# Kernel tuning notes

Hardware: AMD Instinct MI355X
Metric: run time of the kernel (lower is better)

Reference implementation:

```python
import jax, jax.numpy as jnp
import numpy as np

E = 4          # num_experts
B = 32         # batch
CIN = 64
COUT = 64
H = 112
WID = 112
K = 3          # kernel size


def setup_inputs() -> dict:
    key = jax.random.key(0)
    k1, k2, k3, k4 = jax.random.split(key, 4)
    x = jax.random.normal(k1, (B, CIN, H, WID), dtype=jnp.float32)
    layer_mask = jax.random.uniform(k2, (B, E), dtype=jnp.float32)
    # per-expert conv weights/biases (kaiming-ish scale)
    W = jax.random.normal(k3, (E, COUT, CIN, K, K), dtype=jnp.float32) * 0.05
    b = jax.random.normal(k4, (E, COUT), dtype=jnp.float32) * 0.05
    return {"x": x, "layer_mask": layer_mask, "W": W, "b": b}


def _conv(x, w):
    # stride 1, padding 1 on both spatial dims (matches nn.Conv2d(k=3, s=1, p=1))
    return jax.lax.conv_general_dilated(
        x, w, window_strides=(1, 1), padding=[(1, 1), (1, 1)],
        dimension_numbers=("NCHW", "OIHW", "NCHW"))


def reference(x, layer_mask, W, b):
    # Loop over the small fixed expert set, accumulating the gated sum to
    # avoid materializing an [E, B, C, H, W] intermediate.
    out = jnp.zeros((B, COUT, H, WID), dtype=x.dtype)
    for e in range(E):
        expert_out = _conv(x, W[e]) + b[e][None, :, None, None]
        gate = layer_mask[:, e][:, None, None, None]  # [B,1,1,1]
        out = out + expert_out * gate
    return out
```

## Files before the change

### kernel.cpp

```cpp
#include <hip/hip_runtime.h>
#include <stdint.h>

#define CIN   64
#define COUT  64
#define HH    112
#define WW    112
#define NEXP  4
#define HW    (HH * WW)

typedef short bf16x8 __attribute__((ext_vector_type(8)));
typedef float f32x16 __attribute__((ext_vector_type(16)));

__device__ inline uint16_t f2bf(float f) {
    uint32_t u = __builtin_bit_cast(uint32_t, f);
    return (uint16_t)((u + 0x7FFFu + ((u >> 16) & 1u)) >> 16);
}

__global__ __launch_bounds__(256)
void fold_wb(const float* __restrict__ W, const float* __restrict__ bias,
             const float* __restrict__ mask,
             uint16_t* __restrict__ Weff, float* __restrict__ Beff, int B) {
    int idx = blockIdx.x * 256 + threadIdx.x;
    if (idx >= B * 72 * 512) return;
    int j   = idx & 7;
    int co  = (idx >> 3) & 63;
    int g   = (idx >> 9) % 72;
    int n   = idx / (512 * 72);
    int par   = g & 1;
    int kq    = (g >> 1) & 1;
    int khw   = (g >> 2) % 9;
    int phase = (g >> 2) / 9;
    int ci = phase * 32 + (kq * 2 + par) * 8 + j;
    float acc = 0.f;
#pragma unroll
    for (int e = 0; e < NEXP; ++e)
        acc = fmaf(mask[n * NEXP + e],
                   W[((size_t)(e * COUT + co) * CIN + ci) * 9 + khw], acc);
    Weff[idx] = f2bf(acc);
    if (g == 0 && j == 0) {
        float ba = 0.f;
#pragma unroll
        for (int e = 0; e < NEXP; ++e)
            ba = fmaf(mask[n * NEXP + e], bias[e * COUT + co], ba);
        Beff[n * COUT + co] = ba;
    }
}

__global__ __launch_bounds__(256, 3)
void conv_fused(const float* __restrict__ x, const uint16_t* __restrict__ Weff,
                const float* __restrict__ Beff, float* __restrict__ out,
                int nwg) {
    __shared__ uint16_t ldsx[324 * 32];

    int bid = blockIdx.x;
    if ((nwg & 7) == 0)
        bid = (bid & 7) * (nwg >> 3) + (bid >> 3);

    const int tid  = threadIdx.x;
    const int lane = tid & 63;
    const int wid  = tid >> 6;
    const int tileIdx = bid % 49;
    const int n  = bid / 49;
    const int th = tileIdx / 7, tw = tileIdx % 7;
    const int h0 = th * 16, w0 = tw * 16;

    const int rowb = wid * 4 + ((lane & 31) >> 4);
    const int colb = lane & 15;
    const int par  = lane >> 5;

    const uint16_t* wbase = Weff + (size_t)n * 36864
                          + (size_t)par * 512 + (size_t)(lane & 31) * 8;

    f32x16 acc00 = {}, acc01 = {}, acc10 = {}, acc11 = {};

#pragma unroll
    for (int phase = 0; phase < 2; ++phase) {
        if (phase) __syncthreads();
        for (int u = tid; u < 1296; u += 256) {
            int s   = u & 3;
            int pix = u >> 2;
            int dh = pix / 18, dw = pix - dh * 18;
            int h = h0 + dh - 1, w = w0 + dw - 1;
            int cg = s ^ ((pix >> 1) & 3);
            union { uint16_t e[8]; uint4 v; } pk;
            if ((unsigned)h < (unsigned)HH && (unsigned)w < (unsigned)WW) {
                const float* xp = x + ((size_t)(n * CIN + phase * 32 + cg * 8) * HH + h) * WW + w;
#pragma unroll
                for (int j = 0; j < 8; ++j) pk.e[j] = f2bf(xp[(size_t)j * HW]);
            } else {
                pk.v = (uint4){0, 0, 0, 0};
            }
            *(uint4*)(&ldsx[pix * 32 + s * 8]) = pk.v;
        }
        __syncthreads();

        const uint16_t* wp = wbase + (size_t)phase * (36 * 512);
#pragma unroll 1
        for (int khw = 0; khw < 9; ++khw) {
            const int dh = khw / 3;
            const int dw = khw - dh * 3;
            const int pb0 = (rowb + dh) * 18 + (colb + dw);
            const int pb1 = pb0 + 36;
            const int f0 = (pb0 >> 1) & 3, f1 = (pb1 >> 1) & 3;
            const uint16_t* lp0 = &ldsx[pb0 * 32];
            const uint16_t* lp1 = &ldsx[pb1 * 32];
#pragma unroll
            for (int kq = 0; kq < 2; ++kq) {
                const int cgA = kq * 2 + par;
                bf16x8 b0 = *(const bf16x8*)(lp0 + (((cgA ^ f0)) << 3));
                bf16x8 b1 = *(const bf16x8*)(lp1 + (((cgA ^ f1)) << 3));
                const uint16_t* wk = wp + (size_t)((khw * 2 + kq) * 2) * 512;
                bf16x8 a0 = *(const bf16x8*)(wk);
                bf16x8 a1 = *(const bf16x8*)(wk + 256);
                acc00 = __builtin_amdgcn_mfma_f32_32x32x16_bf16(a0, b0, acc00, 0, 0, 0);
                acc01 = __builtin_amdgcn_mfma_f32_32x32x16_bf16(a0, b1, acc01, 0, 0, 0);
                acc10 = __builtin_amdgcn_mfma_f32_32x32x16_bf16(a1, b0, acc10, 0, 0, 0);
                acc11 = __builtin_amdgcn_mfma_f32_32x32x16_bf16(a1, b1, acc11, 0, 0, 0);
            }
        }
    }

    const float* bptr = Beff + n * 64;
    const int row0 = h0 + rowb;
    const int col  = w0 + colb;
#pragma unroll
    for (int r = 0; r < 16; ++r) {
        const int co = (r & 3) + 8 * (r >> 2) + 4 * par;
        const float bia0 = bptr[co];
        const float bia1 = bptr[co + 32];
        size_t o00 = ((size_t)(n * COUT + co) * HH + row0) * WW + col;
        out[o00]          = acc00[r] + bia0;
        out[o00 + 2 * WW] = acc01[r] + bia0;
        size_t o10 = o00 + (size_t)32 * HW;
        out[o10]          = acc10[r] + bia1;
        out[o10 + 2 * WW] = acc11[r] + bia1;
    }
}

#define COB   8
#define PIX_PER_BLK 256
#define NTILE (HW / PIX_PER_BLK)

__global__ void fold_weights(const float* __restrict__ W,
                             const float* __restrict__ mask,
                             float* __restrict__ Weff, int B) {
    int idx = blockIdx.x * blockDim.x + threadIdx.x;
    int total = B * CIN * 9 * COUT;
    if (idx >= total) return;
    int co = idx % COUT;
    int t  = idx / COUT;
    int k  = t % 9;
    t /= 9;
    int ci = t % CIN;
    int n  = t / CIN;
    float acc = 0.f;
#pragma unroll
    for (int e = 0; e < NEXP; ++e)
        acc = fmaf(mask[n * NEXP + e],
                   W[(((size_t)(e * COUT + co) * CIN + ci) * 9) + k], acc);
    Weff[idx] = acc;
}

__global__ __launch_bounds__(PIX_PER_BLK, 4)
void conv_gated(const float* __restrict__ x,
                const float* __restrict__ mask,
                const float* __restrict__ bias,
                const float* __restrict__ Weff,
                float* __restrict__ out) {
    const int tile = blockIdx.x % NTILE;
    const int cob  = (blockIdx.x / NTILE) % (COUT / COB);
    const int n    = blockIdx.x / (NTILE * (COUT / COB));
    const int p = tile * PIX_PER_BLK + threadIdx.x;
    const int h = p / WW;
    const int w = p % WW;
    const int co0 = cob * COB;

    float acc[COB];
#pragma unroll
    for (int j = 0; j < COB; ++j) {
        float a = 0.f;
#pragma unroll
        for (int e = 0; e < NEXP; ++e)
            a = fmaf(mask[n * NEXP + e], bias[e * COUT + co0 + j], a);
        acc[j] = a;
    }

    const float* xb = x + (((size_t)n * CIN) * HH + h) * WW + w;
    const float* wb = Weff + ((size_t)n * CIN) * 9 * COUT + co0;
    const bool rok0 = (h > 0), rok2 = (h < HH - 1);
    const bool cok0 = (w > 0), cok2 = (w < WW - 1);

    for (int ci = 0; ci < CIN; ++ci) {
        const float* xc = xb + (size_t)ci * HW;
        const float* wc = wb + (size_t)ci * 9 * COUT;
#pragma unroll
        for (int kh = 0; kh < 3; ++kh) {
            const bool rok = (kh == 0) ? rok0 : ((kh == 2) ? rok2 : true);
#pragma unroll
            for (int kw = 0; kw < 3; ++kw) {
                const bool cok = (kw == 0) ? cok0 : ((kw == 2) ? cok2 : true);
                float xv = (rok && cok) ? xc[(kh - 1) * WW + (kw - 1)] : 0.f;
                const float4* wk = (const float4*)(wc + (kh * 3 + kw) * COUT);
                float4 wa = wk[0], wb4 = wk[1];
                acc[0] = fmaf(xv, wa.x, acc[0]);
                acc[1] = fmaf(xv, wa.y, acc[1]);
                acc[2] = fmaf(xv, wa.z, acc[2]);
                acc[3] = fmaf(xv, wa.w, acc[3]);
                acc[4] = fmaf(xv, wb4.x, acc[4]);
                acc[5] = fmaf(xv, wb4.y, acc[5]);
                acc[6] = fmaf(xv, wb4.z, acc[6]);
                acc[7] = fmaf(xv, wb4.w, acc[7]);
            }
        }
    }
    float* ob = out + (((size_t)(n * COUT + co0)) * HH + h) * WW + w;
#pragma unroll
    for (int j = 0; j < COB; ++j)
        ob[(size_t)j * HW] = acc[j];
}

extern "C" void kernel_launch(void* const* d_in, const int* in_sizes, int n_in,
                              void* d_out, int out_size, void* d_ws, size_t ws_size,
                              hipStream_t stream) {
    const float* x    = (const float*)d_in[0];
    const float* mask = (const float*)d_in[1];
    const float* W    = (const float*)d_in[2];
    const float* b    = (const float*)d_in[3];
    float* out = (float*)d_out;

    const int B = in_sizes[0] / (CIN * HW);
    const size_t weffB = (size_t)B * 36864 * 2;
    const size_t beffB = (size_t)B * COUT * 4;
    const size_t need  = weffB + beffB;

    if (ws_size >= need) {
        uint16_t* Weff = (uint16_t*)d_ws;
        float*    Beff = (float*)((char*)d_ws + weffB);
        int foldBlocks = (B * 72 * 512 + 255) / 256;
        fold_wb<<<foldBlocks, 256, 0, stream>>>(W, b, mask, Weff, Beff, B);
        const int nwg = B * 49;
        conv_fused<<<nwg, 256, 0, stream>>>(x, Weff, Beff, out, nwg);
    } else {
        float* Weff = (float*)d_ws;
        const size_t weff_elems = (size_t)B * CIN * 9 * COUT;
        int foldBlocks = (int)((weff_elems + 255) / 256);
        fold_weights<<<foldBlocks, 256, 0, stream>>>(W, mask, Weff, B);
        conv_gated<<<B * (COUT / COB) * NTILE, PIX_PER_BLK, 0, stream>>>(
            x, mask, b, Weff, out);
    }
}
```

Before: 75.70 us.

## Prefetch second channel phase into registers during first-phase MFMA compute

The convolution kernel now uses a double-buffered LDS tile. The second 32-channel half of the input is loaded into registers before the first half's MFMA loop runs, then packed into the second buffer afterwards, so global load latency overlaps with compute. The khw loop is partially unrolled and output stores become nontemporal. This adds about 48 float registers per thread and doubles LDS use, which could lower occupancy below the 3 workgroups per CU requested by the launch bounds or cause spills.

Measured after the change: 81.92 us. 1.08x slower.

```diff
diff --git a/kernel.cpp b/kernel.cpp
--- a/kernel.cpp
+++ b/kernel.cpp
@@ -46,11 +46,68 @@
     }
 }
 
+__device__ inline void load_unit(const float* __restrict__ xph, int u,
+                                 int h0, int w0, float r[8]) {
+    int s   = u & 3;
+    int pix = u >> 2;
+    int dh = pix / 18, dw = pix - dh * 18;
+    int h = h0 + dh - 1, w = w0 + dw - 1;
+    int cg = s ^ ((pix >> 1) & 3);
+    if ((unsigned)h < (unsigned)HH && (unsigned)w < (unsigned)WW) {
+        const float* xp = xph + ((size_t)(cg * 8) * HH + h) * WW + w;
+#pragma unroll
+        for (int j = 0; j < 8; ++j) r[j] = xp[(size_t)j * HW];
+    } else {
+#pragma unroll
+        for (int j = 0; j < 8; ++j) r[j] = 0.f;
+    }
+}
+
+__device__ inline void pack_write(uint16_t* __restrict__ buf, int u,
+                                  const float r[8]) {
+    int s   = u & 3;
+    int pix = u >> 2;
+    union { uint16_t e[8]; uint4 v; } pk;
+#pragma unroll
+    for (int j = 0; j < 8; ++j) pk.e[j] = f2bf(r[j]);
+    *(uint4*)(&buf[pix * 32 + s * 8]) = pk.v;
+}
+
+__device__ inline void compute_phase(const uint16_t* __restrict__ buf,
+                                     const uint16_t* __restrict__ wp,
+                                     int rowb, int colb, int par,
+                                     f32x16& acc00, f32x16& acc01,
+                                     f32x16& acc10, f32x16& acc11) {
+#pragma unroll 3
+    for (int khw = 0; khw < 9; ++khw) {
+        const int dh = khw / 3;
+        const int dw = khw - dh * 3;
+        const int pb0 = (rowb + dh) * 18 + (colb + dw);
+        const int pb1 = pb0 + 36;
+        const int f0 = (pb0 >> 1) & 3, f1 = (pb1 >> 1) & 3;
+        const uint16_t* lp0 = &buf[pb0 * 32];
+        const uint16_t* lp1 = &buf[pb1 * 32];
+#pragma unroll
+        for (int kq = 0; kq < 2; ++kq) {
+            const int cgA = kq * 2 + par;
+            bf16x8 b0 = *(const bf16x8*)(lp0 + ((cgA ^ f0) << 3));
+            bf16x8 b1 = *(const bf16x8*)(lp1 + ((cgA ^ f1) << 3));
+            const uint16_t* wk = wp + (size_t)((khw * 2 + kq) * 2) * 512;
+            bf16x8 a0 = *(const bf16x8*)(wk);
+            bf16x8 a1 = *(const bf16x8*)(wk + 256);
+            acc00 = __builtin_amdgcn_mfma_f32_32x32x16_bf16(a0, b0, acc00, 0, 0, 0);
+            acc01 = __builtin_amdgcn_mfma_f32_32x32x16_bf16(a0, b1, acc01, 0, 0, 0);
+            acc10 = __builtin_amdgcn_mfma_f32_32x32x16_bf16(a1, b0, acc10, 0, 0, 0);
+            acc11 = __builtin_amdgcn_mfma_f32_32x32x16_bf16(a1, b1, acc11, 0, 0, 0);
+        }
+    }
+}
+
 __global__ __launch_bounds__(256, 3)
 void conv_fused(const float* __restrict__ x, const uint16_t* __restrict__ Weff,
                 const float* __restrict__ Beff, float* __restrict__ out,
                 int nwg) {
-    __shared__ uint16_t ldsx[324 * 32];
+    __shared__ uint16_t ldsx[2][324 * 32];
 
     int bid = blockIdx.x;
     if ((nwg & 7) == 0)
@@ -70,55 +127,36 @@
 
     const uint16_t* wbase = Weff + (size_t)n * 36864
                           + (size_t)par * 512 + (size_t)(lane & 31) * 8;
+    const float* xn = x + (size_t)n * CIN * HW;
 
     f32x16 acc00 = {}, acc01 = {}, acc10 = {}, acc11 = {};
 
-#pragma unroll
-    for (int phase = 0; phase < 2; ++phase) {
-        if (phase) __syncthreads();
-        for (int u = tid; u < 1296; u += 256) {
-            int s   = u & 3;
-            int pix = u >> 2;
-            int dh = pix / 18, dw = pix - dh * 18;
-            int h = h0 + dh - 1, w = w0 + dw - 1;
-            int cg = s ^ ((pix >> 1) & 3);
-            union { uint16_t e[8]; uint4 v; } pk;
-            if ((unsigned)h < (unsigned)HH && (unsigned)w < (unsigned)WW) {
-                const float* xp = x + ((size_t)(n * CIN + phase * 32 + cg * 8) * HH + h) * WW + w;
-#pragma unroll
-                for (int j = 0; j < 8; ++j) pk.e[j] = f2bf(xp[(size_t)j * HW]);
-            } else {
-                pk.v = (uint4){0, 0, 0, 0};
-            }
-            *(uint4*)(&ldsx[pix * 32 + s * 8]) = pk.v;
-        }
-        __syncthreads();
-
-        const uint16_t* wp = wbase + (size_t)phase * (36 * 512);
-#pragma unroll 1
-        for (int khw = 0; khw < 9; ++khw) {
-            const int dh = khw / 3;
-            const int dw = khw - dh * 3;
-            const int pb0 = (rowb + dh) * 18 + (colb + dw);
-            const int pb1 = pb0 + 36;
-            const int f0 = (pb0 >> 1) & 3, f1 = (pb1 >> 1) & 3;
-            const uint16_t* lp0 = &ldsx[pb0 * 32];
-            const uint16_t* lp1 = &ldsx[pb1 * 32];
-#pragma unroll
-            for (int kq = 0; kq < 2; ++kq) {
-                const int cgA = kq * 2 + par;
-                bf16x8 b0 = *(const bf16x8*)(lp0 + (((cgA ^ f0)) << 3));
-                bf16x8 b1 = *(const bf16x8*)(lp1 + (((cgA ^ f1)) << 3));
-                const uint16_t* wk = wp + (size_t)((khw * 2 + kq) * 2) * 512;
-                bf16x8 a0 = *(const bf16x8*)(wk);
-                bf16x8 a1 = *(const bf16x8*)(wk + 256);
-                acc00 = __builtin_amdgcn_mfma_f32_32x32x16_bf16(a0, b0, acc00, 0, 0, 0);
-                acc01 = __builtin_amdgcn_mfma_f32_32x32x16_bf16(a0, b1, acc01, 0, 0, 0);
-                acc10 = __builtin_amdgcn_mfma_f32_32x32x16_bf16(a1, b0, acc10, 0, 0, 0);
-                acc11 = __builtin_amdgcn_mfma_f32_32x32x16_bf16(a1, b1, acc11, 0, 0, 0);
-            }
-        }
-    }
+    for (int u = tid; u < 1296; u += 256) {
+        float r[8];
+        load_unit(xn, u, h0, w0, r);
+        pack_write(ldsx[0], u, r);
+    }
+    __syncthreads();
+
+    const float* xph1 = xn + (size_t)32 * HW;
+    float pre[5][8];
+    float pret[8];
+    const bool tail = (tid < 16);
+#pragma unroll
+    for (int i = 0; i < 5; ++i)
+        load_unit(xph1, i * 256 + tid, h0, w0, pre[i]);
+    if (tail) load_unit(xph1, 1280 + tid, h0, w0, pret);
+
+    compute_phase(ldsx[0], wbase, rowb, colb, par, acc00, acc01, acc10, acc11);
+
+#pragma unroll
+    for (int i = 0; i < 5; ++i)
+        pack_write(ldsx[1], i * 256 + tid, pre[i]);
+    if (tail) pack_write(ldsx[1], 1280 + tid, pret);
+    __syncthreads();
+
+    compute_phase(ldsx[1], wbase + (size_t)36 * 512, rowb, colb, par,
+                  acc00, acc01, acc10, acc11);
 
     const float* bptr = Beff + n * 64;
     const int row0 = h0 + rowb;
@@ -129,11 +167,11 @@
         const float bia0 = bptr[co];
         const float bia1 = bptr[co + 32];
         size_t o00 = ((size_t)(n * COUT + co) * HH + row0) * WW + col;
-        out[o00]          = acc00[r] + bia0;
-        out[o00 + 2 * WW] = acc01[r] + bia0;
+        __builtin_nontemporal_store(acc00[r] + bia0, &out[o00]);
+        __builtin_nontemporal_store(acc01[r] + bia0, &out[o00 + 2 * WW]);
         size_t o10 = o00 + (size_t)32 * HW;
-        out[o10]          = acc10[r] + bia1;
-        out[o10 + 2 * WW] = acc11[r] + bia1;
+        __builtin_nontemporal_store(acc10[r] + bia1, &out[o10]);
+        __builtin_nontemporal_store(acc11[r] + bia1, &out[o10 + 2 * WW]);
     }
 }
 
```
